# Optimization experiments

Hardware: AMD Instinct MI355X
Metric: run time of the kernel (lower is better)

## Reference

```python
import jax, jax.numpy as jnp
import numpy as np
import math

HIDDEN = 1024
HEADS = 16
HEAD_DIM = HIDDEN // HEADS
RANK = 16
LORA_SCALING = 1.0 / RANK  # loralib default lora_alpha=1 -> scaling = alpha/r


def setup_inputs() -> dict:
    key = jax.random.key(0)
    ks = jax.random.split(key, 16)
    bs, seq = 4, 2048
    inp = {
        "hidden_states": jax.random.normal(ks[0], (bs, seq, HIDDEN), dtype=jnp.float32),
        "attention_mask": jnp.zeros((bs, 1, 1, seq), dtype=jnp.float32),
    }
    s = 0.02
    for i, nm in enumerate(["q", "k", "v"]):
        inp[f"W{nm}"] = jax.random.normal(ks[1 + 4 * i], (HIDDEN, HIDDEN), dtype=jnp.float32) * s
        inp[f"b{nm}"] = jnp.zeros((HIDDEN,), dtype=jnp.float32)
        inp[f"A{nm}"] = jax.random.normal(ks[2 + 4 * i], (RANK, HIDDEN), dtype=jnp.float32) * s
        inp[f"B{nm}"] = jnp.zeros((HIDDEN, RANK), dtype=jnp.float32)  # loralib inits B to zero
    return inp


def _lora_linear(x, W, b, A, B):
    # y = x W^T + b + scaling * (x A^T) B^T
    return x @ W.T + b + LORA_SCALING * ((x @ A.T) @ B.T)


def _transform(x, W, b, A, B, bs, seq):
    proj = _lora_linear(x, W, b, A, B)  # [bs, seq, hidden]
    return proj.reshape(bs, seq, HEADS, HEAD_DIM).transpose(0, 2, 1, 3)  # [bs, h, seq, d]


def reference(hidden_states, attention_mask, Wq, bq, Aq, Bq, Wk, bk, Ak, Bk, Wv, bv, Av, Bv):
    bs, seq, _ = hidden_states.shape
    q = _transform(hidden_states, Wq, bq, Aq, Bq, bs, seq)
    k = _transform(hidden_states, Wk, bk, Ak, Bk, bs, seq)
    v = _transform(hidden_states, Wv, bv, Av, Bv, bs, seq)
    scores = jnp.einsum("bhqd,bhkd->bhqk", q, k) / math.sqrt(HEAD_DIM) + attention_mask
    probs = jax.nn.softmax(scores, axis=-1)  # [bs, h, seq, seq]
    out = jnp.einsum("bhqk,bhkd->bhqd", probs, v)  # [bs, h, seq, d]
    return out.transpose(0, 2, 1, 3).reshape(bs, seq, HIDDEN)
```

## Files before the change

### kernel.cpp

```cpp
#include <hip/hip_runtime.h>
#include <stdint.h>

typedef __bf16 bf16x8 __attribute__((ext_vector_type(8)));
typedef float f32x4 __attribute__((ext_vector_type(4)));
typedef float f32x16 __attribute__((ext_vector_type(16)));

static __device__ __forceinline__ unsigned short f2bf(float f) {
  unsigned int x = __float_as_uint(f);
  unsigned int r = (x + 0x7fffu + ((x >> 16) & 1u)) >> 16;
  return (unsigned short)r;
}
static __device__ __forceinline__ unsigned int pk_bf16(float a, float b) {
  unsigned int d;
  asm("v_cvt_pk_bf16_f32 %0, %1, %2" : "=v"(d) : "v"(a), "v"(b));
  return d;
}
static __device__ __forceinline__ float exp2_hw(float x) {
  float r;
  asm("v_exp_f32 %0, %1" : "=v"(r) : "v"(x));
  return r;
}
static __device__ __forceinline__ float rcp_hw(float x) {
  float r;
  asm("v_rcp_f32 %0, %1" : "=v"(r) : "v"(x));
  return r;
}

static __device__ __forceinline__ void gll16(const void* g, void* l) {
  __builtin_amdgcn_global_load_lds((const __attribute__((address_space(1))) unsigned int*)g,
                                   (__attribute__((address_space(3))) unsigned int*)l,
                                   16, 0, 0);
}

__global__ __launch_bounds__(256) void convert_x(const float* __restrict__ X,
                                                 unsigned short* __restrict__ Xbf) {
  int i = (blockIdx.x * 256 + threadIdx.x) * 4;
  float4 v = *(const float4*)(X + i);
  uint2 o;
  o.x = pk_bf16(v.x, v.y);
  o.y = pk_bf16(v.z, v.w);
  *(uint2*)(Xbf + i) = o;
}

__global__ __launch_bounds__(256) void build_weff(
    const float* __restrict__ Wq, const float* __restrict__ Aq, const float* __restrict__ Bq,
    const float* __restrict__ Wk, const float* __restrict__ Ak, const float* __restrict__ Bk,
    const float* __restrict__ Wv, const float* __restrict__ Av, const float* __restrict__ Bv,
    unsigned short* __restrict__ Weff) {
  int idx = blockIdx.x * 256 + threadIdx.x;
  int p = idx >> 20;
  int o = (idx >> 10) & 1023;
  int i = idx & 1023;
  const float* W = (p == 0) ? Wq : (p == 1) ? Wk : Wv;
  const float* A = (p == 0) ? Aq : (p == 1) ? Ak : Av;
  const float* B = (p == 0) ? Bq : (p == 1) ? Bk : Bv;
  float acc = 0.f;
#pragma unroll
  for (int r = 0; r < 16; ++r)
    acc += B[o * 16 + r] * A[r * 1024 + i];
  Weff[idx] = f2bf(W[o * 1024 + i] + acc * 0.0625f);
}

__global__ __launch_bounds__(256) void gemm_qkv(
    const unsigned short* __restrict__ X, const unsigned short* __restrict__ Weff,
    const float* __restrict__ bq, const float* __restrict__ bk, const float* __restrict__ bv,
    unsigned short* __restrict__ qbuf, unsigned short* __restrict__ kbuf,
    unsigned short* __restrict__ vtbuf) {
  __shared__ __align__(16) unsigned short As[128][32];
  __shared__ __align__(16) unsigned short Bs[128][32];
  const int K = 1024;
  int tid = threadIdx.x;
  int lane = tid & 63;
  int w = tid >> 6;
  int wm = (w >> 1) * 64;
  int wn = (w & 1) * 64;
  int c = lane & 15;
  int quad = lane >> 4;
  int m0 = blockIdx.y * 128;
  int n0 = blockIdx.x * 128;
  int p = n0 >> 10;

  int ldrow = lane >> 2;
  int ldcol = (lane & 3) * 8;
  const unsigned short* gA = X + (m0 + w * 32 + ldrow) * K + ldcol;
  const unsigned short* gB = Weff + (n0 + w * 32 + ldrow) * K + ldcol;

  f32x4 acc[4][4] = {};

  if (p == 2) {
    for (int k0 = 0; k0 < K; k0 += 32) {
      __syncthreads();
      gll16(gA + k0, &As[w * 32][0]);
      gll16(gA + 16 * K + k0, &As[w * 32 + 16][0]);
      gll16(gB + k0, &Bs[w * 32][0]);
      gll16(gB + 16 * K + k0, &Bs[w * 32 + 16][0]);
      __syncthreads();
      bf16x8 af[4], bfr[4];
#pragma unroll
      for (int mi = 0; mi < 4; mi++)
        af[mi] = *(const bf16x8*)&As[wm + mi * 16 + c][quad * 8];
#pragma unroll
      for (int ni = 0; ni < 4; ni++)
        bfr[ni] = *(const bf16x8*)&Bs[wn + ni * 16 + c][quad * 8];
#pragma unroll
      for (int mi = 0; mi < 4; mi++)
#pragma unroll
        for (int ni = 0; ni < 4; ni++)
          acc[mi][ni] = __builtin_amdgcn_mfma_f32_16x16x32_bf16(af[mi], bfr[ni], acc[mi][ni], 0, 0, 0);
    }
    const float* bias = bv;
#pragma unroll
    for (int ni = 0; ni < 4; ni++) {
      int o = (n0 + wn + ni * 16 + c) & 1023;
      int h = o >> 6;
      int d = o & 63;
      float bval = bias[o];
#pragma unroll
      for (int mi = 0; mi < 4; mi++) {
        int mbase = m0 + wm + mi * 16 + quad * 4;
        int bb = mbase >> 11;
        int s = mbase & 2047;
        uint2 o4;
        o4.x = pk_bf16(acc[mi][ni][0] + bval, acc[mi][ni][1] + bval);
        o4.y = pk_bf16(acc[mi][ni][2] + bval, acc[mi][ni][3] + bval);
        *(uint2*)&vtbuf[((bb * 16 + h) * 64 + d) * 2048 + s] = o4;
      }
    }
  } else {
    for (int k0 = 0; k0 < K; k0 += 32) {
      __syncthreads();
      gll16(gA + k0, &As[w * 32][0]);
      gll16(gA + 16 * K + k0, &As[w * 32 + 16][0]);
      gll16(gB + k0, &Bs[w * 32][0]);
      gll16(gB + 16 * K + k0, &Bs[w * 32 + 16][0]);
      __syncthreads();
      bf16x8 af[4], bfr[4];
#pragma unroll
      for (int mi = 0; mi < 4; mi++)
        af[mi] = *(const bf16x8*)&As[wm + mi * 16 + c][quad * 8];
#pragma unroll
      for (int ni = 0; ni < 4; ni++)
        bfr[ni] = *(const bf16x8*)&Bs[wn + ni * 16 + c][quad * 8];
#pragma unroll
      for (int mi = 0; mi < 4; mi++)
#pragma unroll
        for (int ni = 0; ni < 4; ni++)
          acc[mi][ni] = __builtin_amdgcn_mfma_f32_16x16x32_bf16(bfr[ni], af[mi], acc[mi][ni], 0, 0, 0);
    }
    const float* bias = (p == 1) ? bk : bq;
    unsigned short* dst = (p == 1) ? kbuf : qbuf;
#pragma unroll
    for (int mi = 0; mi < 4; mi++) {
      int m = m0 + wm + mi * 16 + c;
      int bb = m >> 11;
      int ss = m & 2047;
#pragma unroll
      for (int ni = 0; ni < 4; ni++) {
        int o = (n0 + wn + ni * 16 + quad * 4) & 1023;
        int h = o >> 6;
        int d = o & 63;
        float4 b4 = *(const float4*)&bias[o];
        uint2 o4;
        o4.x = pk_bf16(acc[mi][ni][0] + b4.x, acc[mi][ni][1] + b4.y);
        o4.y = pk_bf16(acc[mi][ni][2] + b4.z, acc[mi][ni][3] + b4.w);
        *(uint2*)&dst[((bb * 16 + h) * 2048 + ss) * 64 + d] = o4;
      }
    }
  }
}

__global__ __launch_bounds__(256) void attn_kernel(
    const unsigned short* __restrict__ qbuf, const unsigned short* __restrict__ kbuf,
    const unsigned short* __restrict__ vtbuf, const float* __restrict__ maskg,
    float* __restrict__ out) {
  __shared__ __align__(16) unsigned short Qs[128][72];
  __shared__ __align__(16) unsigned short Ks[64][72];
  __shared__ __align__(16) unsigned short Vts[64][72];
  __shared__ __align__(16) unsigned short Ps[4][32][72];
  __shared__ __align__(16) float masks2[64];
  __shared__ __align__(16) float lrow[128];

  const float SC = 0.125f * 1.4426950408889634f;

  int tid = threadIdx.x;
  int lane = tid & 63;
  int w = tid >> 6;
  int m31 = lane & 31;
  int hi = lane >> 5;
  int bh = blockIdx.y;
  int b = bh >> 4;
  int h = bh & 15;
  int q0 = blockIdx.x * 128;

  const unsigned short* Qbh = qbuf + bh * (2048 * 64);
  const unsigned short* Kbh = kbuf + bh * (2048 * 64);
  const unsigned short* Vbh = vtbuf + bh * (64 * 2048);

  int r2 = tid >> 3;
  int ch = (tid & 7) * 8;

#pragma unroll
  for (int ps = 0; ps < 4; ps++)
    *(uint4*)&Qs[ps * 32 + r2][ch] = *(const uint4*)(Qbh + (q0 + ps * 32 + r2) * 64 + ch);

  float lsum = 0.f;
  f32x16 acc_o[2] = {};

  for (int kt = 0; kt < 2048; kt += 64) {
    __syncthreads();
#pragma unroll
    for (int ps = 0; ps < 2; ps++) {
      *(uint4*)&Ks[ps * 32 + r2][ch] = *(const uint4*)(Kbh + (kt + ps * 32 + r2) * 64 + ch);
      *(uint4*)&Vts[ps * 32 + r2][ch] = *(const uint4*)(Vbh + (ps * 32 + r2) * 2048 + kt + ch);
    }
    if (tid < 64) masks2[tid] = (maskg[b * 2048 + kt + tid] - 8.0f) * 1.4426950408889634f;
    __syncthreads();

    f32x16 accs[2] = {};
#pragma unroll
    for (int ks = 0; ks < 4; ks++) {
      bf16x8 qf = *(const bf16x8*)&Qs[w * 32 + m31][ks * 16 + hi * 8];
#pragma unroll
      for (int kb = 0; kb < 2; kb++) {
        bf16x8 kf = *(const bf16x8*)&Ks[kb * 32 + m31][ks * 16 + hi * 8];
        accs[kb] = __builtin_amdgcn_mfma_f32_32x32x16_bf16(kf, qf, accs[kb], 0, 0, 0);
      }
    }

#pragma unroll
    for (int kb = 0; kb < 2; kb++)
#pragma unroll
      for (int g = 0; g < 4; g++) {
        float4 m4 = *(const float4*)&masks2[kb * 32 + g * 8 + hi * 4];
        float p0 = exp2_hw(fmaf(accs[kb][g * 4 + 0], SC, m4.x));
        float p1 = exp2_hw(fmaf(accs[kb][g * 4 + 1], SC, m4.y));
        float p2 = exp2_hw(fmaf(accs[kb][g * 4 + 2], SC, m4.z));
        float p3 = exp2_hw(fmaf(accs[kb][g * 4 + 3], SC, m4.w));
        lsum += (p0 + p1) + (p2 + p3);
        uint2 pk2;
        pk2.x = pk_bf16(p0, p1);
        pk2.y = pk_bf16(p2, p3);
        *(uint2*)&Ps[w][m31][kb * 32 + g * 8 + hi * 4] = pk2;
      }
    __asm__ volatile("" ::: "memory");

#pragma unroll
    for (int ks = 0; ks < 4; ks++) {
      bf16x8 pf = *(const bf16x8*)&Ps[w][m31][ks * 16 + hi * 8];
#pragma unroll
      for (int db = 0; db < 2; db++) {
        bf16x8 vf = *(const bf16x8*)&Vts[db * 32 + m31][ks * 16 + hi * 8];
        acc_o[db] = __builtin_amdgcn_mfma_f32_32x32x16_bf16(pf, vf, acc_o[db], 0, 0, 0);
      }
    }
  }

  lsum += __shfl_xor(lsum, 32);
  lrow[w * 32 + m31] = lsum;
  __asm__ volatile("" ::: "memory");

#pragma unroll
  for (int g = 0; g < 4; g++) {
    float4 l4 = *(const float4*)&lrow[w * 32 + g * 8 + hi * 4];
    float i0 = rcp_hw(l4.x), i1 = rcp_hw(l4.y), i2 = rcp_hw(l4.z), i3 = rcp_hw(l4.w);
#pragma unroll
    for (int db = 0; db < 2; db++) {
      int qq = q0 + w * 32 + g * 8 + hi * 4;
      float* obase = out + (b * 2048 + qq) * 1024 + h * 64 + db * 32 + m31;
      obase[0 * 1024] = acc_o[db][g * 4 + 0] * i0;
      obase[1 * 1024] = acc_o[db][g * 4 + 1] * i1;
      obase[2 * 1024] = acc_o[db][g * 4 + 2] * i2;
      obase[3 * 1024] = acc_o[db][g * 4 + 3] * i3;
    }
  }
}

extern "C" void kernel_launch(void* const* d_in, const int* in_sizes, int n_in,
                              void* d_out, int out_size, void* d_ws, size_t ws_size,
                              hipStream_t stream) {
  const float* X    = (const float*)d_in[0];
  const float* mask = (const float*)d_in[1];
  const float* Wq = (const float*)d_in[2];
  const float* bq = (const float*)d_in[3];
  const float* Aq = (const float*)d_in[4];
  const float* Bq = (const float*)d_in[5];
  const float* Wk = (const float*)d_in[6];
  const float* bk = (const float*)d_in[7];
  const float* Ak = (const float*)d_in[8];
  const float* Bk = (const float*)d_in[9];
  const float* Wv = (const float*)d_in[10];
  const float* bv = (const float*)d_in[11];
  const float* Av = (const float*)d_in[12];
  const float* Bv = (const float*)d_in[13];

  unsigned short* ws    = (unsigned short*)d_ws;
  unsigned short* Xbf   = ws;
  unsigned short* Weff  = Xbf + 8388608;
  unsigned short* qbuf  = Weff + 3145728;
  unsigned short* kbuf  = qbuf + 8388608;
  unsigned short* vtbuf = kbuf + 8388608;

  convert_x<<<dim3(8192), dim3(256), 0, stream>>>(X, Xbf);
  build_weff<<<dim3(12288), dim3(256), 0, stream>>>(Wq, Aq, Bq, Wk, Ak, Bk, Wv, Av, Bv, Weff);
  gemm_qkv<<<dim3(24, 64), dim3(256), 0, stream>>>(Xbf, Weff, bq, bk, bv, qbuf, kbuf, vtbuf);
  attn_kernel<<<dim3(16, 64), dim3(256), 0, stream>>>(qbuf, kbuf, vtbuf, mask, (float*)d_out);
}
```

Before: 321.4 us.

## Keep softmax probabilities in registers instead of LDS round-trip for PV MFMA

Removes the per-warp shared-memory P buffer and feeds the bf16-packed probabilities directly from registers into the PV matrix multiply. It uses the older 32x32x8 bf16 MFMA, whose operand layout matches the accumulator layout, when that builtin is available. Otherwise it falls back to cross-half lane shuffles that rebuild the 32x32x16 operand. It also adds a min-blocks-per-CU launch bound of 4, which caps register use and may cause spills. The goal is to cut LDS write/read traffic and the associated waits, at the cost of twice as many smaller MFMAs on the x8 path.

Result: faster. 296.9 us (-7.6%).

```diff
diff --git a/kernel.cpp b/kernel.cpp
--- a/kernel.cpp
+++ b/kernel.cpp
@@ -4,6 +4,9 @@
 typedef __bf16 bf16x8 __attribute__((ext_vector_type(8)));
 typedef float f32x4 __attribute__((ext_vector_type(4)));
 typedef float f32x16 __attribute__((ext_vector_type(16)));
+typedef short s16x4 __attribute__((ext_vector_type(4)));
+
+#define HAS_X8 __has_builtin(__builtin_amdgcn_mfma_f32_32x32x8bf16_1k)
 
 static __device__ __forceinline__ unsigned short f2bf(float f) {
   unsigned int x = __float_as_uint(f);
@@ -169,14 +172,13 @@
   }
 }
 
-__global__ __launch_bounds__(256) void attn_kernel(
+__global__ __launch_bounds__(256, 4) void attn_kernel(
     const unsigned short* __restrict__ qbuf, const unsigned short* __restrict__ kbuf,
     const unsigned short* __restrict__ vtbuf, const float* __restrict__ maskg,
     float* __restrict__ out) {
   __shared__ __align__(16) unsigned short Qs[128][72];
   __shared__ __align__(16) unsigned short Ks[64][72];
   __shared__ __align__(16) unsigned short Vts[64][72];
-  __shared__ __align__(16) unsigned short Ps[4][32][72];
   __shared__ __align__(16) float masks2[64];
   __shared__ __align__(16) float lrow[128];
 
@@ -227,6 +229,7 @@
       }
     }
 
+    unsigned int up[2][4][2];
 #pragma unroll
     for (int kb = 0; kb < 2; kb++)
 #pragma unroll
@@ -237,22 +240,48 @@
         float p2 = exp2_hw(fmaf(accs[kb][g * 4 + 2], SC, m4.z));
         float p3 = exp2_hw(fmaf(accs[kb][g * 4 + 3], SC, m4.w));
         lsum += (p0 + p1) + (p2 + p3);
-        uint2 pk2;
-        pk2.x = pk_bf16(p0, p1);
-        pk2.y = pk_bf16(p2, p3);
-        *(uint2*)&Ps[w][m31][kb * 32 + g * 8 + hi * 4] = pk2;
-      }
-    __asm__ volatile("" ::: "memory");
-
-#pragma unroll
-    for (int ks = 0; ks < 4; ks++) {
-      bf16x8 pf = *(const bf16x8*)&Ps[w][m31][ks * 16 + hi * 8];
+        up[kb][g][0] = pk_bf16(p0, p1);
+        up[kb][g][1] = pk_bf16(p2, p3);
+      }
+
+#if HAS_X8
+#pragma unroll
+    for (int kb = 0; kb < 2; kb++)
+#pragma unroll
+      for (int g = 0; g < 4; g++) {
+        union { uint2 u; s16x4 s; } pc;
+        pc.u.x = up[kb][g][0];
+        pc.u.y = up[kb][g][1];
+        int col = kb * 32 + g * 8 + hi * 4;
+#pragma unroll
+        for (int db = 0; db < 2; db++) {
+          union { uint2 u; s16x4 s; } vc;
+          vc.u = *(const uint2*)&Vts[db * 32 + m31][col];
+          acc_o[db] = __builtin_amdgcn_mfma_f32_32x32x8bf16_1k(pc.s, vc.s, acc_o[db], 0, 0, 0);
+        }
+      }
+#else
+#pragma unroll
+    for (int s = 0; s < 4; s++) {
+      int kb = s >> 1, g0 = (s & 1) * 2, g1 = g0 + 1;
+      unsigned int A0 = up[kb][g0][0], A1 = up[kb][g0][1];
+      unsigned int B0 = up[kb][g1][0], B1 = up[kb][g1][1];
+      unsigned int A0x = (unsigned int)__shfl_xor((int)A0, 32);
+      unsigned int A1x = (unsigned int)__shfl_xor((int)A1, 32);
+      unsigned int B0x = (unsigned int)__shfl_xor((int)B0, 32);
+      unsigned int B1x = (unsigned int)__shfl_xor((int)B1, 32);
+      union { uint4 u; bf16x8 bv8; } pf;
+      pf.u.x = hi ? B0x : A0;
+      pf.u.y = hi ? B1x : A1;
+      pf.u.z = hi ? B0 : A0x;
+      pf.u.w = hi ? B1 : A1x;
 #pragma unroll
       for (int db = 0; db < 2; db++) {
-        bf16x8 vf = *(const bf16x8*)&Vts[db * 32 + m31][ks * 16 + hi * 8];
-        acc_o[db] = __builtin_amdgcn_mfma_f32_32x32x16_bf16(pf, vf, acc_o[db], 0, 0, 0);
-      }
-    }
+        bf16x8 vf = *(const bf16x8*)&Vts[db * 32 + m31][s * 16 + hi * 8];
+        acc_o[db] = __builtin_amdgcn_mfma_f32_32x32x16_bf16(pf.bv8, vf, acc_o[db], 0, 0, 0);
+      }
+    }
+#endif
   }
 
   lsum += __shfl_xor(lsum, 32);
```
